# Performance work log

Hardware: AMD Instinct MI355X
Metric: run time of the kernel (lower is better)

Reference implementation:

```python
import jax, jax.numpy as jnp
import numpy as np


def setup_inputs() -> dict:
    key = jax.random.key(0)
    k0, k1, k2, k3 = jax.random.split(key, 4)
    B, S, D, F, E = 8, 2048, 1024, 2048, 8
    x = jax.random.normal(k0, (B, S, D), dtype=jnp.float32)
    Wg = jax.random.normal(k1, (D, E), dtype=jnp.float32) * 0.02
    W1 = jax.random.normal(k2, (E, D, F), dtype=jnp.float32) * 0.02
    W2 = jax.random.normal(k3, (E, F, D), dtype=jnp.float32) * 0.02
    return {"x": x, "Wg": Wg, "W1": W1, "W2": W2}


def reference(x, Wg, W1, W2):
    # Expert-choice MoE: experts pick top-C tokens, conflicts resolved by
    # max router prob (ties -> lowest expert index, matching the serial loop).
    B, S, D = x.shape
    E = Wg.shape[1]
    T = B * S
    cap = max(1, T // E)  # capacity_factor = 1.0

    xt = x.reshape(T, D)
    logits = xt @ Wg                      # [T, E]
    probs = jax.nn.softmax(logits, axis=-1)
    pT = probs.T                          # [E, T] token affinities per expert

    _, top_idx = jax.lax.top_k(pT, cap)   # [E, cap] tokens chosen by each expert
    sel = jnp.zeros((E, T), dtype=bool).at[jnp.arange(E)[:, None], top_idx].set(True)

    # Serial conflict loop is equivalent to: per token, pick the selecting
    masked = jnp.where(sel, pT, -jnp.inf)
    assigned = sel.any(axis=0)            # [T]
    tok2exp = jnp.where(assigned,
                        jnp.argmax(masked, axis=0),
                        jnp.argmax(pT, axis=0))          # [T] int
    weights = jnp.take_along_axis(probs, tok2exp[:, None], axis=1)[:, 0]  # [T]

    # Dispatch / expert FFN / weighted combine. Loop over the small fixed
    # expert set; masked tokens contribute exactly zero, matching index_add_.
    out = jnp.zeros_like(xt)
    for e in range(E):
        gate = jnp.where(tok2exp == e, weights, 0.0)     # [T]
        h = jax.nn.gelu(xt @ W1[e], approximate=False) @ W2[e]  # [T, D]
        out = out + gate[:, None] * h

    return out.reshape(B, S, D)
```

## Files before the change

### kernel.cpp

```cpp
#include <hip/hip_runtime.h>
#include <hip/hip_bf16.h>
#include <math.h>

#define T_TOK 16384
#define DIM   1024
#define FF    2048
#define NE    8
#define CAPK  2048
#define MTE_MAX 16
#define WL1SZ (NE * 8 * MTE_MAX)
#define WL2SZ (NE * 4 * MTE_MAX)

typedef unsigned short u16;
typedef unsigned long long u64;
typedef __attribute__((ext_vector_type(8))) short bf16x8;
typedef __attribute__((ext_vector_type(4))) float f32x4;

__device__ __forceinline__ u16 f2bf(float f) {
  __hip_bfloat16 h = __float2bfloat16(f);
  union { __hip_bfloat16 h; u16 u; } c; c.h = h; return c.u;
}

__device__ __forceinline__ float gelu_f(float v) {
  float z = fabsf(v) * 0.70710678118654752f;
  float t = __builtin_amdgcn_rcpf(1.0f + 0.3275911f * z);
  float poly = t * (0.254829592f +
               t * (-0.284496736f +
               t * (1.421413741f +
               t * (-1.453152027f +
               t * 1.061405429f))));
  float ez = __expf(-z * z);
  float erfz = 1.0f - poly * ez;
  erfz = copysignf(erfz, v);
  return 0.5f * v * (1.0f + erfz);
}

__device__ __forceinline__ void async_copy16(const void* g, void* l) {
  __builtin_amdgcn_global_load_lds(
      (const __attribute__((address_space(1))) unsigned int*)g,
      (__attribute__((address_space(3))) unsigned int*)l, 16, 0, 0);
}

__device__ __forceinline__ bf16x8 ds_read16(const char* p) {
  bf16x8 r;
  asm volatile("ds_read_b128 %0, %1"
               : "=&v"(r)
               : "v"((const __attribute__((address_space(3))) char*)p));
  return r;
}

__global__ __launch_bounds__(256) void transpose_cvt2(const float* __restrict__ W1,
                                                      const float* __restrict__ W2,
                                                      u16* __restrict__ w1t,
                                                      u16* __restrict__ w2t) {
  __shared__ float tile[64][65];
  int z = blockIdx.y;
  const float* src;
  u16* dst;
  int R, C;
  if (z < 8) { src = W1 + (size_t)z * DIM * FF; dst = w1t + (size_t)z * DIM * FF; R = DIM; C = FF; }
  else       { src = W2 + (size_t)(z - 8) * FF * DIM; dst = w2t + (size_t)(z - 8) * FF * DIM; R = FF; C = DIM; }
  int nbx = C >> 6;
  int bx = blockIdx.x % nbx, by = blockIdx.x / nbx;
  int r0 = by * 64, c0 = bx * 64;
  int tid = threadIdx.x;
  int lr = tid >> 4, lc4 = (tid & 15) * 4;
#pragma unroll
  for (int p = 0; p < 4; ++p) {
    float4 v = *(const float4*)(src + (size_t)(r0 + p * 16 + lr) * C + c0 + lc4);
    tile[p * 16 + lr][lc4 + 0] = v.x;
    tile[p * 16 + lr][lc4 + 1] = v.y;
    tile[p * 16 + lr][lc4 + 2] = v.z;
    tile[p * 16 + lr][lc4 + 3] = v.w;
  }
  __syncthreads();
  int oc = tid >> 3, orr = (tid & 7) * 8;
#pragma unroll
  for (int p = 0; p < 2; ++p) {
    int c = p * 32 + oc;
    u16 h[8];
#pragma unroll
    for (int j = 0; j < 8; ++j) h[j] = f2bf(tile[orr + j][c]);
    *(uint4*)(dst + (size_t)(c0 + c) * R + r0 + orr) = *(uint4*)h;
  }
}

__global__ __launch_bounds__(256) void router_k(const float* __restrict__ x,
                                                const float* __restrict__ Wg,
                                                float* __restrict__ probs,
                                                float* __restrict__ probsT,
                                                u16* __restrict__ xb,
                                                u64* __restrict__ key,
                                                int* cnt, int* cnt2) {
  int tid = threadIdx.x;
  if (tid < 4) key[blockIdx.x * 4 + tid] = 0ull;
  if (blockIdx.x == 0 && tid < NE) { cnt[tid] = 0; cnt2[tid] = 0; }
  int wid = tid >> 6, lane = tid & 63;
  int t = blockIdx.x * 4 + wid;
  const float* xr = x + (size_t)t * DIM;
  u16* xbr = xb + (size_t)t * DIM;
  double acc[NE] = {0, 0, 0, 0, 0, 0, 0, 0};
#pragma unroll 1
  for (int it = 0; it < DIM / 64; ++it) {
    int d = it * 64 + lane;
    float xv = xr[d];
    xbr[d] = f2bf(xv);
    const float4* wrow = (const float4*)(Wg + (size_t)d * NE);
    float4 w0 = wrow[0], w1 = wrow[1];
    acc[0] += (double)xv * (double)w0.x;
    acc[1] += (double)xv * (double)w0.y;
    acc[2] += (double)xv * (double)w0.z;
    acc[3] += (double)xv * (double)w0.w;
    acc[4] += (double)xv * (double)w1.x;
    acc[5] += (double)xv * (double)w1.y;
    acc[6] += (double)xv * (double)w1.z;
    acc[7] += (double)xv * (double)w1.w;
  }
#pragma unroll
  for (int e = 0; e < NE; ++e)
    for (int o = 32; o > 0; o >>= 1) acc[e] += __shfl_down(acc[e], o, 64);
  if (lane == 0) {
    float l[NE], mx = -3.0e38f;
#pragma unroll
    for (int e = 0; e < NE; ++e) { l[e] = (float)acc[e]; mx = fmaxf(mx, l[e]); }
    float s = 0.f;
#pragma unroll
    for (int e = 0; e < NE; ++e) { l[e] = expf(l[e] - mx); s += l[e]; }
    float inv = 1.0f / s;
#pragma unroll
    for (int e = 0; e < NE; ++e) {
      float p = l[e] * inv;
      probs[(size_t)t * NE + e] = p;
      probsT[(size_t)e * T_TOK + t] = p;
    }
  }
}

__global__ __launch_bounds__(256) void topk_sel(const float* __restrict__ probsT,
                                                u64* __restrict__ key) {
  __shared__ float pcol[T_TOK];
  __shared__ unsigned whist[8][2048];
  __shared__ unsigned hist[2048];
  __shared__ unsigned bcast[2];
  __shared__ unsigned wsum[4];
  __shared__ int wps[4];
  int e = blockIdx.x, tid = threadIdx.x, wid = tid >> 6, lane = tid & 63;
  const float4* src4 = (const float4*)(probsT + (size_t)e * T_TOK);
  for (int i = tid; i < T_TOK / 4; i += 256) ((float4*)pcol)[i] = src4[i];
  for (int i = tid; i < 8 * 2048; i += 256) ((unsigned*)whist)[i] = 0;
  unsigned prefix = 0, remaining = CAPK;
#pragma unroll 1
  for (int lvl = 0; lvl < 3; ++lvl) {
    int nb = (lvl == 2) ? 1024 : 2048;
    if (lvl == 0) {
      __syncthreads();
      for (int i = tid; i < T_TOK; i += 256)
        atomicAdd(&whist[wid][__float_as_uint(pcol[i]) >> 21], 1u);
      __syncthreads();
      for (int j = tid; j < 2048; j += 256) {
        unsigned s2 = 0;
#pragma unroll
        for (int w = 0; w < 8; ++w) s2 += whist[w][j];
        hist[j] = s2;
      }
      __syncthreads();
    } else {
      for (int i = tid; i < 2048; i += 256) hist[i] = 0;
      __syncthreads();
      for (int i = tid; i < T_TOK; i += 256) {
        unsigned k = __float_as_uint(pcol[i]);
        bool m = (lvl == 1) ? ((k >> 21) == prefix) : ((k >> 10) == prefix);
        if (m) atomicAdd(&hist[(lvl == 1) ? ((k >> 10) & 2047u) : (k & 1023u)], 1u);
      }
      __syncthreads();
    }
    int nper = nb / 256;
    unsigned cv = 0;
    for (int j = 0; j < nper; ++j) cv += hist[tid * nper + j];
    unsigned s = cv;
#pragma unroll
    for (int o = 1; o < 64; o <<= 1) {
      unsigned tv = __shfl_down(s, o, 64);
      if (lane + o < 64) s += tv;
    }
    if (lane == 0) wsum[wid] = s;
    __syncthreads();
    unsigned above = 0;
    for (int w = wid + 1; w < 4; ++w) above += wsum[w];
    unsigned Sincl = s + above, Sexcl = Sincl - cv;
    if (Sincl >= remaining && Sexcl < remaining) {
      unsigned rem2 = remaining - Sexcl, cum2 = 0;
      for (int j = nper - 1; j >= 0; --j) {
        unsigned h = hist[tid * nper + j];
        if (cum2 + h >= rem2) { bcast[0] = (unsigned)(tid * nper + j); bcast[1] = rem2 - cum2; break; }
        cum2 += h;
      }
    }
    __syncthreads();
    unsigned b = bcast[0];
    remaining = bcast[1];
    prefix = (lvl == 0) ? b : (lvl == 1) ? ((prefix << 11) | b) : ((prefix << 10) | b);
    __syncthreads();
  }
  unsigned vk = prefix;
  int need = (int)remaining;
  const int CH = T_TOK / 256;
  int i0 = tid * CH;
  int myt = 0;
  for (int i = i0; i < i0 + CH; ++i)
    myt += (__float_as_uint(pcol[i]) == vk);
  int p = myt;
#pragma unroll
  for (int o = 1; o < 64; o <<= 1) {
    int tv = __shfl_up(p, o, 64);
    if (lane >= o) p += tv;
  }
  if (lane == 63) wps[wid] = p;
  __syncthreads();
  int wo = 0;
  for (int w = 0; w < wid; ++w) wo += wps[w];
  int run = wo + p - myt;
  u64 ebits = (u64)(7 - e);
  for (int i = i0; i < i0 + CH; ++i) {
    unsigned k = __float_as_uint(pcol[i]);
    bool sv = false;
    if (k > vk) sv = true;
    else if (k == vk) { if (run < need) sv = true; run++; }
    if (sv) atomicMax(&key[i], ((u64)k << 3) | ebits);
  }
}

__global__ __launch_bounds__(256) void assign_k(const float* __restrict__ probs,
                                                const u64* __restrict__ key,
                                                int* __restrict__ tok2exp,
                                                float* __restrict__ wgt, int* cnt) {
  int t = blockIdx.x * 256 + threadIdx.x;
  int lane = threadIdx.x & 63;
  u64 k = key[t];
  int best;
  float bp;
  if (k) {
    best = 7 - (int)(k & 7);
    bp = __uint_as_float((unsigned)(k >> 3));
  } else {
    best = 0; bp = -3.0e38f;
#pragma unroll
    for (int e = 0; e < NE; ++e) {
      float p = probs[(size_t)t * NE + e];
      if (p > bp) { bp = p; best = e; }
    }
  }
  tok2exp[t] = best;
  wgt[t] = bp;
#pragma unroll
  for (int e = 0; e < NE; ++e) {
    u64 m = __ballot(best == e);
    if (best == e && lane == __ffsll(m) - 1) atomicAdd(&cnt[e], (int)__popcll(m));
  }
}

__global__ __launch_bounds__(256) void slot_wl_k(const int* __restrict__ tok2exp,
                                                 const int* __restrict__ cnt,
                                                 int* cnt2, int* __restrict__ list,
                                                 int* basep, int* wl1, int* wl2) {
  int gid = blockIdx.x * 256 + threadIdx.x;
  int lane = threadIdx.x & 63;
  int c[NE];
#pragma unroll
  for (int e = 0; e < NE; ++e) c[e] = cnt[e];
  if (gid < NE) {
    int r = 0;
    for (int e = 0; e < gid; ++e) r += c[e];
    basep[gid] = r;
  }
  if (gid < WL1SZ) {
    int e = gid & 7, j = gid >> 3;
    int mte = (c[e] + 255) >> 8;
    int v = -1;
    if (j < 8 * mte) {
      int half = 4 * mte;
      int h = (j >= half) ? 1 : 0;
      int jj = j - h * half;
      v = e | ((jj >> 2) << 4) | (((h << 2) | (jj & 3)) << 12);
    }
    wl1[gid] = v;
  }
  if (gid >= WL1SZ && gid < WL1SZ + WL2SZ) {
    int g2 = gid - WL1SZ;
    int e = g2 & 7, j = g2 >> 3;
    int mte = (c[e] + 255) >> 8;
    int v = -1;
    if (j < 4 * mte) {
      int half = 2 * mte;
      int h = (j >= half) ? 1 : 0;
      int jj = j - h * half;
      v = e | ((jj >> 1) << 4) | (((h << 1) | (jj & 1)) << 12);
    }
    wl2[g2] = v;
  }
  int te = tok2exp[gid];
  int bp_e = 0;
#pragma unroll
  for (int e = 0; e < NE; ++e) if (e < te) bp_e += c[e];
  int sl = 0;
#pragma unroll
  for (int e = 0; e < NE; ++e) {
    u64 m = __ballot(te == e);
    if (te == e) {
      int leader = __ffsll(m) - 1;
      int rank = __popcll(m & ((1ull << lane) - 1));
      int b = 0;
      if (lane == leader) b = atomicAdd(&cnt2[e], (int)__popcll(m));
      b = __shfl(b, leader, 64);
      sl = bp_e + b + rank;
    }
  }
  list[sl] = gid;
}


#define MF(M, N_, AV, BV) acc[M][N_] = __builtin_amdgcn_mfma_f32_16x16x32_bf16(BV, AV, acc[M][N_], 0, 0, 0)

#define SLOT_A(s) (sm + (s) * 32768)
#define SLOT_B(s) (sm + (s) * 32768 + 16384)

#define DSA_LO(s)                                                                 \
  pa = SLOT_A(s) + wr * 8192 + laneOff;                                           \
  a0 = ds_read16(pa);        a1 = ds_read16(pa + 1024);                           \
  a2 = ds_read16(pa + 2048); a3 = ds_read16(pa + 3072);

#define DSA_HI(s)                                                                 \
  pa = SLOT_A(s) + wr * 8192 + 4096 + laneOff;                                    \
  a4 = ds_read16(pa);        a5 = ds_read16(pa + 1024);                           \
  a6 = ds_read16(pa + 2048); a7 = ds_read16(pa + 3072);

#define DSB_RD(s, BP)                                                             \
  pb = SLOT_B(s) + wc * 4096 + laneOff;                                           \
  BP##0 = ds_read16(pb);        BP##1 = ds_read16(pb + 1024);                     \
  BP##2 = ds_read16(pb + 2048); BP##3 = ds_read16(pb + 3072);

#define LGKM(n)                                                                   \
  do {                                                                            \
    asm volatile("s_waitcnt lgkmcnt(" #n ")" ::: "memory");                       \
    __builtin_amdgcn_sched_barrier(0);                                            \
  } while (0)

#define VMW(n) asm volatile("s_waitcnt vmcnt(" #n ")" ::: "memory")
#define BAR() asm volatile("s_barrier" ::: "memory")

#define MFMA_LO(BP)                                                               \
  do {                                                                            \
    __builtin_amdgcn_s_setprio(1);                                                \
    MF(0, 0, a0, BP##0); MF(0, 1, a0, BP##1); MF(0, 2, a0, BP##2); MF(0, 3, a0, BP##3); \
    MF(1, 0, a1, BP##0); MF(1, 1, a1, BP##1); MF(1, 2, a1, BP##2); MF(1, 3, a1, BP##3); \
    MF(2, 0, a2, BP##0); MF(2, 1, a2, BP##1); MF(2, 2, a2, BP##2); MF(2, 3, a2, BP##3); \
    MF(3, 0, a3, BP##0); MF(3, 1, a3, BP##1); MF(3, 2, a3, BP##2); MF(3, 3, a3, BP##3); \
    __builtin_amdgcn_s_setprio(0);                                                \
  } while (0)

#define MFMA_HI(BP)                                                               \
  do {                                                                            \
    __builtin_amdgcn_s_setprio(1);                                                \
    MF(4, 0, a4, BP##0); MF(4, 1, a4, BP##1); MF(4, 2, a4, BP##2); MF(4, 3, a4, BP##3); \
    MF(5, 0, a5, BP##0); MF(5, 1, a5, BP##1); MF(5, 2, a5, BP##2); MF(5, 3, a5, BP##3); \
    MF(6, 0, a6, BP##0); MF(6, 1, a6, BP##1); MF(6, 2, a6, BP##2); MF(6, 3, a6, BP##3); \
    MF(7, 0, a7, BP##0); MF(7, 1, a7, BP##1); MF(7, 2, a7, BP##2); MF(7, 3, a7, BP##3); \
    __builtin_amdgcn_s_setprio(0);                                                \
  } while (0)

#define STAGE_A(s, kt)                                                            \
  do {                                                                            \
    async_copy16(aP0 + (size_t)(kt) * 64, SLOT_A(s) + wid * 1024);                \
    async_copy16(aP1 + (size_t)(kt) * 64, SLOT_A(s) + 8192 + wid * 1024);         \
  } while (0)

#define STAGE_B(s, kt)                                                            \
  do {                                                                            \
    async_copy16(bP0 + (size_t)(kt) * 64, SLOT_B(s) + wid * 1024);                \
    async_copy16(bP1 + (size_t)(kt) * 64, SLOT_B(s) + 8192 + wid * 1024);         \
  } while (0)

#define TILE_KT(kt, BCUR, BNXT)                                                   \
  do {                                                                            \
    const int sC = (kt) & 3, sP = ((kt) + 3) & 3, sN = ((kt) + 1) & 3;            \
    if ((kt) + 3 < KT) STAGE_A(sP, (kt) + 3);                                     \
    DSA_HI(sC);                                                                   \
    LGKM(4);                                                                      \
    MFMA_LO(BCUR);                                                                \
    if ((kt) + 3 < KT) STAGE_B(sP, (kt) + 3);                                     \
    if ((kt) < KT - 1) {                                                          \
      if ((kt) < KT - 3)        { VMW(8); }                                       \
      else if ((kt) == KT - 3)  { VMW(4); }                                       \
      else                      { VMW(0); }                                       \
      BAR();                                                                      \
      DSB_RD(sN, BNXT);                                                           \
      DSA_LO(sN);                                                                 \
      LGKM(8);                                                                    \
    } else {                                                                      \
      LGKM(0);                                                                    \
    }                                                                             \
    MFMA_HI(BCUR);                                                                \
  } while (0)

template <int EPI>
__global__ __launch_bounds__(512, 2) void ffn_k(const u16* __restrict__ A,
                                                const u16* __restrict__ Bm,
                                                void* __restrict__ Out,
                                                const int* __restrict__ list,
                                                const float* __restrict__ wgt,
                                                const int* __restrict__ basep,
                                                const int* __restrict__ cnt,
                                                const int* __restrict__ wl) {
  constexpr int K = EPI ? FF : DIM;
  constexpr int N = EPI ? DIM : FF;
  constexpr int KT = K / 32;

  const int wle = wl[blockIdx.x];
  if (wle < 0) return;
  const int e = wle & 15, mt = (wle >> 4) & 255, nt = wle >> 12;
  const int ce = cnt[e];
  const int be = basep[e];

  __shared__ u16 smem[65536];
  __shared__ int toks[256];
  __shared__ float wsc[256];
  char* const sm = (char*)smem;

  const int tid = threadIdx.x;
  if (tid < 256) {
    int r = mt * 256 + tid;
    int tk = (r < ce) ? list[be + r] : list[be];
    toks[tid] = tk;
    if (EPI == 1) wsc[tid] = wgt[tk];
  }
  __syncthreads();

  const int wid = tid >> 6, lane = tid & 63;
  const int wr = wid >> 2, wc = wid & 3;
  const int laneOff = ((lane & 15) >> 1) * 128 + (lane & 1) * 64 +
                      (((lane >> 4) << 4) ^ (((lane >> 1) & 3) << 4));

  const int tr0 = ((tid >> 3) << 1) + ((tid >> 2) & 1), tr1 = 128 + tr0;
  const int cbl = ((tid & 3) << 4) ^ (((tid >> 3) & 3) << 4);
  const char *aP0, *aP1;
  if (EPI == 0) {
    aP0 = (const char*)(A + (size_t)toks[tr0] * K) + cbl;
    aP1 = (const char*)(A + (size_t)toks[tr1] * K) + cbl;
  } else {
    aP0 = (const char*)(A + ((size_t)be + mt * 256 + tr0) * K) + cbl;
    aP1 = (const char*)(A + ((size_t)be + mt * 256 + tr1) * K) + cbl;
  }
  const char* bP0 = (const char*)(Bm + ((size_t)e * N + nt * 256 + tr0) * K) + cbl;
  const char* bP1 = (const char*)(Bm + ((size_t)e * N + nt * 256 + tr1) * K) + cbl;

  f32x4 acc[8][4];
#pragma unroll
  for (int m = 0; m < 8; ++m)
#pragma unroll
    for (int n = 0; n < 4; ++n) acc[m][n] = (f32x4){0.f, 0.f, 0.f, 0.f};

  STAGE_A(0, 0); STAGE_B(0, 0);
  STAGE_A(1, 1); STAGE_B(1, 1);
  STAGE_A(2, 2); STAGE_B(2, 2);
  VMW(8);
  BAR();

  const char* pa;
  const char* pb;
  bf16x8 a0, a1, a2, a3, a4, a5, a6, a7;
  bf16x8 bA0, bA1, bA2, bA3, bB0, bB1, bB2, bB3;

  DSB_RD(0, bA);
  DSA_LO(0);

#pragma unroll 1
  for (int kt = 0; kt < KT; kt += 2) {
    TILE_KT(kt, bA, bB);
    TILE_KT(kt + 1, bB, bA);
  }

  const int lc = lane & 15, lq = (lane >> 4) * 4;
#pragma unroll
  for (int m = 0; m < 8; ++m) {
    int trow = wr * 128 + m * 16 + lc;
    int grow = mt * 256 + trow;
    if (grow < ce) {
      if (EPI == 0) {
        size_t rowoff = (size_t)(be + grow) * FF + nt * 256 + wc * 64 + lq;
#pragma unroll
        for (int n = 0; n < 4; ++n) {
          ushort4 h4;
          h4.x = f2bf(gelu_f(acc[m][n][0]));
          h4.y = f2bf(gelu_f(acc[m][n][1]));
          h4.z = f2bf(gelu_f(acc[m][n][2]));
          h4.w = f2bf(gelu_f(acc[m][n][3]));
          *(ushort4*)((u16*)Out + rowoff + n * 16) = h4;
        }
      } else {
        float w = wsc[trow];
        size_t rowoff = (size_t)toks[trow] * DIM + nt * 256 + wc * 64 + lq;
#pragma unroll
        for (int n = 0; n < 4; ++n) {
          float4 o = make_float4(w * acc[m][n][0], w * acc[m][n][1],
                                 w * acc[m][n][2], w * acc[m][n][3]);
          *(float4*)((float*)Out + rowoff + n * 16) = o;
        }
      }
    }
  }
}

extern "C" void kernel_launch(void* const* d_in, const int* in_sizes, int n_in,
                              void* d_out, int out_size, void* d_ws, size_t ws_size,
                              hipStream_t stream) {
  (void)in_sizes; (void)n_in; (void)out_size; (void)ws_size;
  const float* x  = (const float*)d_in[0];
  const float* Wg = (const float*)d_in[1];
  const float* W1 = (const float*)d_in[2];
  const float* W2 = (const float*)d_in[3];
  float* out = (float*)d_out;

  char* ws = (char*)d_ws;
  size_t off = 0;
  auto alloc = [&](size_t bytes) -> void* {
    void* p = ws + off;
    off += (bytes + 255) & ~(size_t)255;
    return p;
  };
  u16* xb   = (u16*)alloc((size_t)T_TOK * DIM * 2);
  u16* w1t  = (u16*)alloc((size_t)NE * FF * DIM * 2);
  u16* w2t  = (u16*)alloc((size_t)NE * DIM * FF * 2);
  u16* H    = (u16*)alloc((size_t)(T_TOK + 256) * FF * 2);
  float* probs  = (float*)alloc((size_t)T_TOK * NE * 4);
  float* probsT = (float*)alloc((size_t)NE * T_TOK * 4);
  u64* key      = (u64*)alloc((size_t)T_TOK * 8);
  float* wgt    = (float*)alloc((size_t)T_TOK * 4);
  int* tok2exp  = (int*)alloc((size_t)T_TOK * 4);
  int* list     = (int*)alloc((size_t)T_TOK * 4);
  int* cnt      = (int*)alloc(64);
  int* cnt2     = (int*)alloc(64);
  int* basep    = (int*)alloc(64);
  int* wl1      = (int*)alloc(WL1SZ * 4);
  int* wl2      = (int*)alloc(WL2SZ * 4);

  transpose_cvt2<<<dim3(512, 16), 256, 0, stream>>>(W1, W2, w1t, w2t);
  router_k<<<T_TOK / 4, 256, 0, stream>>>(x, Wg, probs, probsT, xb, key, cnt, cnt2);
  topk_sel<<<NE, 256, 0, stream>>>(probsT, key);
  assign_k<<<T_TOK / 256, 256, 0, stream>>>(probs, key, tok2exp, wgt, cnt);
  slot_wl_k<<<T_TOK / 256, 256, 0, stream>>>(tok2exp, cnt, cnt2, list, basep, wl1, wl2);
  ffn_k<0><<<WL1SZ, 512, 0, stream>>>(xb, w1t, H, list, wgt, basep, cnt, wl1);
  ffn_k<1><<<WL2SZ, 512, 0, stream>>>(H, w2t, out, list, wgt, basep, cnt, wl2);
}
```

Measured before the change: 386.7 us.

## Merge prep and routing kernels, shrink FFN GEMM tiles to 128x128 double-buffered

```diff
diff --git a/kernel.cpp b/kernel.cpp
--- a/kernel.cpp
+++ b/kernel.cpp
@@ -7,9 +7,8 @@
 #define FF    2048
 #define NE    8
 #define CAPK  2048
-#define MTE_MAX 16
-#define WL1SZ (NE * 8 * MTE_MAX)
-#define WL2SZ (NE * 4 * MTE_MAX)
+#define WL1SZ 4096
+#define WL2SZ 2048
 
 typedef unsigned short u16;
 typedef unsigned long long u64;
@@ -49,361 +48,325 @@
   return r;
 }
 
-__global__ __launch_bounds__(256) void transpose_cvt2(const float* __restrict__ W1,
-                                                      const float* __restrict__ W2,
-                                                      u16* __restrict__ w1t,
-                                                      u16* __restrict__ w2t) {
+#define LGKM0()                                                                   \
+  do {                                                                            \
+    asm volatile("s_waitcnt lgkmcnt(0)" ::: "memory");                            \
+    __builtin_amdgcn_sched_barrier(0);                                            \
+  } while (0)
+#define VMW0() asm volatile("s_waitcnt vmcnt(0)" ::: "memory")
+#define BAR() asm volatile("s_barrier" ::: "memory")
+
+__global__ __launch_bounds__(256) void prep_k(const float* __restrict__ x,
+                                              const float* __restrict__ Wg,
+                                              const float* __restrict__ W1,
+                                              const float* __restrict__ W2,
+                                              float* __restrict__ probs,
+                                              float* __restrict__ probsT,
+                                              u16* __restrict__ xb,
+                                              u16* __restrict__ w1t,
+                                              u16* __restrict__ w2t,
+                                              u64* __restrict__ key,
+                                              int* cnt, int* cnt2, int* gates) {
   __shared__ float tile[64][65];
-  int z = blockIdx.y;
-  const float* src;
-  u16* dst;
-  int R, C;
-  if (z < 8) { src = W1 + (size_t)z * DIM * FF; dst = w1t + (size_t)z * DIM * FF; R = DIM; C = FF; }
-  else       { src = W2 + (size_t)(z - 8) * FF * DIM; dst = w2t + (size_t)(z - 8) * FF * DIM; R = FF; C = DIM; }
-  int nbx = C >> 6;
-  int bx = blockIdx.x % nbx, by = blockIdx.x / nbx;
-  int r0 = by * 64, c0 = bx * 64;
-  int tid = threadIdx.x;
-  int lr = tid >> 4, lc4 = (tid & 15) * 4;
-#pragma unroll
-  for (int p = 0; p < 4; ++p) {
-    float4 v = *(const float4*)(src + (size_t)(r0 + p * 16 + lr) * C + c0 + lc4);
-    tile[p * 16 + lr][lc4 + 0] = v.x;
-    tile[p * 16 + lr][lc4 + 1] = v.y;
-    tile[p * 16 + lr][lc4 + 2] = v.z;
-    tile[p * 16 + lr][lc4 + 3] = v.w;
+  int bid = blockIdx.x, tid = threadIdx.x;
+  if (bid < 4096) {
+    if (tid < 4) key[bid * 4 + tid] = 0ull;
+    if (bid == 0 && tid < NE) { cnt[tid] = 0; cnt2[tid] = 0; }
+    if (bid == 0 && tid >= 8 && tid < 10) gates[tid - 8] = 0;
+    int wid = tid >> 6, lane = tid & 63;
+    int t = bid * 4 + wid;
+    const float* xr = x + (size_t)t * DIM;
+    u16* xbr = xb + (size_t)t * DIM;
+    double acc[NE] = {0, 0, 0, 0, 0, 0, 0, 0};
+#pragma unroll 1
+    for (int it = 0; it < DIM / 64; ++it) {
+      int d = it * 64 + lane;
+      float xv = xr[d];
+      xbr[d] = f2bf(xv);
+      const float4* wrow = (const float4*)(Wg + (size_t)d * NE);
+      float4 w0 = wrow[0], w1 = wrow[1];
+      acc[0] += (double)xv * (double)w0.x;
+      acc[1] += (double)xv * (double)w0.y;
+      acc[2] += (double)xv * (double)w0.z;
+      acc[3] += (double)xv * (double)w0.w;
+      acc[4] += (double)xv * (double)w1.x;
+      acc[5] += (double)xv * (double)w1.y;
+      acc[6] += (double)xv * (double)w1.z;
+      acc[7] += (double)xv * (double)w1.w;
+    }
+#pragma unroll
+    for (int e = 0; e < NE; ++e)
+      for (int o = 32; o > 0; o >>= 1) acc[e] += __shfl_down(acc[e], o, 64);
+    if (lane == 0) {
+      float l[NE], mx = -3.0e38f;
+#pragma unroll
+      for (int e = 0; e < NE; ++e) { l[e] = (float)acc[e]; mx = fmaxf(mx, l[e]); }
+      float s = 0.f;
+#pragma unroll
+      for (int e = 0; e < NE; ++e) { l[e] = expf(l[e] - mx); s += l[e]; }
+      float inv = 1.0f / s;
+#pragma unroll
+      for (int e = 0; e < NE; ++e) {
+        float p = l[e] * inv;
+        probs[(size_t)t * NE + e] = p;
+        probsT[(size_t)e * T_TOK + t] = p;
+      }
+    }
+  } else {
+    int tz = bid - 4096;
+    int z = tz >> 9, bxy = tz & 511;
+    const float* src;
+    u16* dst;
+    int R, C;
+    if (z < 8) { src = W1 + (size_t)z * DIM * FF; dst = w1t + (size_t)z * DIM * FF; R = DIM; C = FF; }
+    else       { src = W2 + (size_t)(z - 8) * FF * DIM; dst = w2t + (size_t)(z - 8) * FF * DIM; R = FF; C = DIM; }
+    int nbx = C >> 6;
+    int bx = bxy % nbx, by = bxy / nbx;
+    int r0 = by * 64, c0 = bx * 64;
+    int lr = tid >> 4, lc4 = (tid & 15) * 4;
+#pragma unroll
+    for (int p = 0; p < 4; ++p) {
+      float4 v = *(const float4*)(src + (size_t)(r0 + p * 16 + lr) * C + c0 + lc4);
+      tile[p * 16 + lr][lc4 + 0] = v.x;
+      tile[p * 16 + lr][lc4 + 1] = v.y;
+      tile[p * 16 + lr][lc4 + 2] = v.z;
+      tile[p * 16 + lr][lc4 + 3] = v.w;
+    }
+    __syncthreads();
+    int oc = tid >> 3, orr = (tid & 7) * 8;
+#pragma unroll
+    for (int p = 0; p < 2; ++p) {
+      int c = p * 32 + oc;
+      u16 h[8];
+#pragma unroll
+      for (int j = 0; j < 8; ++j) h[j] = f2bf(tile[orr + j][c]);
+      *(uint4*)(dst + (size_t)(c0 + c) * R + r0 + orr) = *(uint4*)h;
+    }
   }
-  __syncthreads();
-  int oc = tid >> 3, orr = (tid & 7) * 8;
-#pragma unroll
-  for (int p = 0; p < 2; ++p) {
-    int c = p * 32 + oc;
-    u16 h[8];
-#pragma unroll
-    for (int j = 0; j < 8; ++j) h[j] = f2bf(tile[orr + j][c]);
-    *(uint4*)(dst + (size_t)(c0 + c) * R + r0 + orr) = *(uint4*)h;
-  }
-}
-
-__global__ __launch_bounds__(256) void router_k(const float* __restrict__ x,
-                                                const float* __restrict__ Wg,
-                                                float* __restrict__ probs,
-                                                float* __restrict__ probsT,
-                                                u16* __restrict__ xb,
-                                                u64* __restrict__ key,
-                                                int* cnt, int* cnt2) {
-  int tid = threadIdx.x;
-  if (tid < 4) key[blockIdx.x * 4 + tid] = 0ull;
-  if (blockIdx.x == 0 && tid < NE) { cnt[tid] = 0; cnt2[tid] = 0; }
-  int wid = tid >> 6, lane = tid & 63;
-  int t = blockIdx.x * 4 + wid;
-  const float* xr = x + (size_t)t * DIM;
-  u16* xbr = xb + (size_t)t * DIM;
-  double acc[NE] = {0, 0, 0, 0, 0, 0, 0, 0};
-#pragma unroll 1
-  for (int it = 0; it < DIM / 64; ++it) {
-    int d = it * 64 + lane;
-    float xv = xr[d];
-    xbr[d] = f2bf(xv);
-    const float4* wrow = (const float4*)(Wg + (size_t)d * NE);
-    float4 w0 = wrow[0], w1 = wrow[1];
-    acc[0] += (double)xv * (double)w0.x;
-    acc[1] += (double)xv * (double)w0.y;
-    acc[2] += (double)xv * (double)w0.z;
-    acc[3] += (double)xv * (double)w0.w;
-    acc[4] += (double)xv * (double)w1.x;
-    acc[5] += (double)xv * (double)w1.y;
-    acc[6] += (double)xv * (double)w1.z;
-    acc[7] += (double)xv * (double)w1.w;
-  }
-#pragma unroll
-  for (int e = 0; e < NE; ++e)
-    for (int o = 32; o > 0; o >>= 1) acc[e] += __shfl_down(acc[e], o, 64);
-  if (lane == 0) {
-    float l[NE], mx = -3.0e38f;
-#pragma unroll
-    for (int e = 0; e < NE; ++e) { l[e] = (float)acc[e]; mx = fmaxf(mx, l[e]); }
-    float s = 0.f;
-#pragma unroll
-    for (int e = 0; e < NE; ++e) { l[e] = expf(l[e] - mx); s += l[e]; }
-    float inv = 1.0f / s;
-#pragma unroll
-    for (int e = 0; e < NE; ++e) {
-      float p = l[e] * inv;
-      probs[(size_t)t * NE + e] = p;
-      probsT[(size_t)e * T_TOK + t] = p;
-    }
-  }
-}
-
-__global__ __launch_bounds__(256) void topk_sel(const float* __restrict__ probsT,
-                                                u64* __restrict__ key) {
+}
+
+__global__ __launch_bounds__(256) void moe_route_k(const float* __restrict__ probsT,
+                                                   const float* __restrict__ probs,
+                                                   u64* __restrict__ key,
+                                                   int* __restrict__ tok2exp,
+                                                   float* __restrict__ wgt,
+                                                   int* cnt, int* cnt2,
+                                                   int* __restrict__ list,
+                                                   int* basep, int* wl1, int* wl2,
+                                                   int* gates) {
   __shared__ float pcol[T_TOK];
   __shared__ unsigned whist[8][2048];
   __shared__ unsigned hist[2048];
   __shared__ unsigned bcast[2];
   __shared__ unsigned wsum[4];
   __shared__ int wps[4];
-  int e = blockIdx.x, tid = threadIdx.x, wid = tid >> 6, lane = tid & 63;
-  const float4* src4 = (const float4*)(probsT + (size_t)e * T_TOK);
-  for (int i = tid; i < T_TOK / 4; i += 256) ((float4*)pcol)[i] = src4[i];
-  for (int i = tid; i < 8 * 2048; i += 256) ((unsigned*)whist)[i] = 0;
-  unsigned prefix = 0, remaining = CAPK;
+  int bid = blockIdx.x, tid = threadIdx.x, wid = tid >> 6, lane = tid & 63;
+  if (bid < 8) {
+    int e = bid;
+    const float4* src4 = (const float4*)(probsT + (size_t)e * T_TOK);
+    for (int i = tid; i < T_TOK / 4; i += 256) ((float4*)pcol)[i] = src4[i];
+    for (int i = tid; i < 8 * 2048; i += 256) ((unsigned*)whist)[i] = 0;
+    unsigned prefix = 0, remaining = CAPK;
 #pragma unroll 1
-  for (int lvl = 0; lvl < 3; ++lvl) {
-    int nb = (lvl == 2) ? 1024 : 2048;
-    if (lvl == 0) {
+    for (int lvl = 0; lvl < 3; ++lvl) {
+      int nb = (lvl == 2) ? 1024 : 2048;
+      if (lvl == 0) {
+        __syncthreads();
+        for (int i = tid; i < T_TOK; i += 256)
+          atomicAdd(&whist[wid][__float_as_uint(pcol[i]) >> 21], 1u);
+        __syncthreads();
+        for (int j = tid; j < 2048; j += 256) {
+          unsigned s2 = 0;
+#pragma unroll
+          for (int w = 0; w < 8; ++w) s2 += whist[w][j];
+          hist[j] = s2;
+        }
+        __syncthreads();
+      } else {
+        for (int i = tid; i < 2048; i += 256) hist[i] = 0;
+        __syncthreads();
+        for (int i = tid; i < T_TOK; i += 256) {
+          unsigned k = __float_as_uint(pcol[i]);
+          bool m = (lvl == 1) ? ((k >> 21) == prefix) : ((k >> 10) == prefix);
+          if (m) atomicAdd(&hist[(lvl == 1) ? ((k >> 10) & 2047u) : (k & 1023u)], 1u);
+        }
+        __syncthreads();
+      }
+      int nper = nb / 256;
+      unsigned cv = 0;
+      for (int j = 0; j < nper; ++j) cv += hist[tid * nper + j];
+      unsigned s = cv;
+#pragma unroll
+      for (int o = 1; o < 64; o <<= 1) {
+        unsigned tv = __shfl_down(s, o, 64);
+        if (lane + o < 64) s += tv;
+      }
+      if (lane == 0) wsum[wid] = s;
       __syncthreads();
-      for (int i = tid; i < T_TOK; i += 256)
-        atomicAdd(&whist[wid][__float_as_uint(pcol[i]) >> 21], 1u);
+      unsigned above = 0;
+      for (int w = wid + 1; w < 4; ++w) above += wsum[w];
+      unsigned Sincl = s + above, Sexcl = Sincl - cv;
+      if (Sincl >= remaining && Sexcl < remaining) {
+        unsigned rem2 = remaining - Sexcl, cum2 = 0;
+        for (int j = nper - 1; j >= 0; --j) {
+          unsigned h = hist[tid * nper + j];
+          if (cum2 + h >= rem2) { bcast[0] = (unsigned)(tid * nper + j); bcast[1] = rem2 - cum2; break; }
+          cum2 += h;
+        }
+      }
       __syncthreads();
-      for (int j = tid; j < 2048; j += 256) {
-        unsigned s2 = 0;
-#pragma unroll
-        for (int w = 0; w < 8; ++w) s2 += whist[w][j];
-        hist[j] = s2;
-      }
+      unsigned b = bcast[0];
+      remaining = bcast[1];
+      prefix = (lvl == 0) ? b : (lvl == 1) ? ((prefix << 11) | b) : ((prefix << 10) | b);
       __syncthreads();
+    }
+    unsigned vk = prefix;
+    int need = (int)remaining;
+    const int CH = T_TOK / 256;
+    int i0 = tid * CH;
+    int myt = 0;
+    for (int i = i0; i < i0 + CH; ++i)
+      myt += (__float_as_uint(pcol[i]) == vk);
+    int p = myt;
+#pragma unroll
+    for (int o = 1; o < 64; o <<= 1) {
+      int tv = __shfl_up(p, o, 64);
+      if (lane >= o) p += tv;
+    }
+    if (lane == 63) wps[wid] = p;
+    __syncthreads();
+    int wo = 0;
+    for (int w = 0; w < wid; ++w) wo += wps[w];
+    int run = wo + p - myt;
+    u64 ebits = (u64)(7 - e);
+    for (int i = i0; i < i0 + CH; ++i) {
+      unsigned k = __float_as_uint(pcol[i]);
+      bool sv = false;
+      if (k > vk) sv = true;
+      else if (k == vk) { if (run < need) sv = true; run++; }
+      if (sv) atomicMax(&key[i], ((u64)k << 3) | ebits);
+    }
+    __threadfence();
+    __syncthreads();
+    if (tid == 0) atomicAdd(&gates[0], 1);
+  } else if (bid < 72) {
+    if (tid == 0) {
+      while (atomicAdd(&gates[0], 0) < 8) __builtin_amdgcn_s_sleep(8);
+    }
+    __syncthreads();
+    __threadfence();
+    int t = (bid - 8) * 256 + tid;
+    u64 k = key[t];
+    int best;
+    float bp;
+    if (k) {
+      best = 7 - (int)(k & 7);
+      bp = __uint_as_float((unsigned)(k >> 3));
     } else {
-      for (int i = tid; i < 2048; i += 256) hist[i] = 0;
-      __syncthreads();
-      for (int i = tid; i < T_TOK; i += 256) {
-        unsigned k = __float_as_uint(pcol[i]);
-        bool m = (lvl == 1) ? ((k >> 21) == prefix) : ((k >> 10) == prefix);
-        if (m) atomicAdd(&hist[(lvl == 1) ? ((k >> 10) & 2047u) : (k & 1023u)], 1u);
-      }
-      __syncthreads();
-    }
-    int nper = nb / 256;
-    unsigned cv = 0;
-    for (int j = 0; j < nper; ++j) cv += hist[tid * nper + j];
-    unsigned s = cv;
-#pragma unroll
-    for (int o = 1; o < 64; o <<= 1) {
-      unsigned tv = __shfl_down(s, o, 64);
-      if (lane + o < 64) s += tv;
-    }
-    if (lane == 0) wsum[wid] = s;
+      best = 0; bp = -3.0e38f;
+#pragma unroll
+      for (int e = 0; e < NE; ++e) {
+        float p = probs[(size_t)t * NE + e];
+        if (p > bp) { bp = p; best = e; }
+      }
+    }
+    tok2exp[t] = best;
+    wgt[t] = bp;
+#pragma unroll
+    for (int e = 0; e < NE; ++e) {
+      u64 m = __ballot(best == e);
+      if (best == e && lane == __ffsll(m) - 1) atomicAdd(&cnt[e], (int)__popcll(m));
+    }
+    __threadfence();
     __syncthreads();
-    unsigned above = 0;
-    for (int w = wid + 1; w < 4; ++w) above += wsum[w];
-    unsigned Sincl = s + above, Sexcl = Sincl - cv;
-    if (Sincl >= remaining && Sexcl < remaining) {
-      unsigned rem2 = remaining - Sexcl, cum2 = 0;
-      for (int j = nper - 1; j >= 0; --j) {
-        unsigned h = hist[tid * nper + j];
-        if (cum2 + h >= rem2) { bcast[0] = (unsigned)(tid * nper + j); bcast[1] = rem2 - cum2; break; }
-        cum2 += h;
-      }
+    if (tid == 0) atomicAdd(&gates[1], 1);
+  } else {
+    if (tid == 0) {
+      while (atomicAdd(&gates[1], 0) < 64) __builtin_amdgcn_s_sleep(8);
     }
     __syncthreads();
-    unsigned b = bcast[0];
-    remaining = bcast[1];
-    prefix = (lvl == 0) ? b : (lvl == 1) ? ((prefix << 11) | b) : ((prefix << 10) | b);
-    __syncthreads();
+    __threadfence();
+    int gid = (bid - 72) * 256 + tid;
+    int c[NE];
+#pragma unroll
+    for (int e = 0; e < NE; ++e) c[e] = cnt[e];
+    if (gid < NE) {
+      int r = 0;
+      for (int e = 0; e < gid; ++e) r += c[e];
+      basep[gid] = r;
+    }
+    if (gid < WL1SZ) {
+      int e = gid & 7, j = gid >> 3;
+      int mte = (c[e] + 127) >> 7;
+      wl1[gid] = (j < mte * 16) ? (e | ((j >> 4) << 4) | ((j & 15) << 12)) : -1;
+    }
+    if (gid >= WL1SZ && gid < WL1SZ + WL2SZ) {
+      int g2 = gid - WL1SZ;
+      int e = g2 & 7, j = g2 >> 3;
+      int mte = (c[e] + 127) >> 7;
+      wl2[g2] = (j < mte * 8) ? (e | ((j >> 3) << 4) | ((j & 7) << 12)) : -1;
+    }
+    int te = tok2exp[gid];
+    int bp_e = 0;
+#pragma unroll
+    for (int e = 0; e < NE; ++e) if (e < te) bp_e += c[e];
+    int sl = 0;
+#pragma unroll
+    for (int e = 0; e < NE; ++e) {
+      u64 m = __ballot(te == e);
+      if (te == e) {
+        int leader = __ffsll(m) - 1;
+        int rank = __popcll(m & ((1ull << lane) - 1));
+        int b = 0;
+        if (lane == leader) b = atomicAdd(&cnt2[e], (int)__popcll(m));
+        b = __shfl(b, leader, 64);
+        sl = bp_e + b + rank;
+      }
+    }
+    list[sl] = gid;
   }
-  unsigned vk = prefix;
-  int need = (int)remaining;
-  const int CH = T_TOK / 256;
-  int i0 = tid * CH;
-  int myt = 0;
-  for (int i = i0; i < i0 + CH; ++i)
-    myt += (__float_as_uint(pcol[i]) == vk);
-  int p = myt;
-#pragma unroll
-  for (int o = 1; o < 64; o <<= 1) {
-    int tv = __shfl_up(p, o, 64);
-    if (lane >= o) p += tv;
-  }
-  if (lane == 63) wps[wid] = p;
-  __syncthreads();
-  int wo = 0;
-  for (int w = 0; w < wid; ++w) wo += wps[w];
-  int run = wo + p - myt;
-  u64 ebits = (u64)(7 - e);
-  for (int i = i0; i < i0 + CH; ++i) {
-    unsigned k = __float_as_uint(pcol[i]);
-    bool sv = false;
-    if (k > vk) sv = true;
-    else if (k == vk) { if (run < need) sv = true; run++; }
-    if (sv) atomicMax(&key[i], ((u64)k << 3) | ebits);
-  }
-}
-
-__global__ __launch_bounds__(256) void assign_k(const float* __restrict__ probs,
-                                                const u64* __restrict__ key,
-                                                int* __restrict__ tok2exp,
-                                                float* __restrict__ wgt, int* cnt) {
-  int t = blockIdx.x * 256 + threadIdx.x;
-  int lane = threadIdx.x & 63;
-  u64 k = key[t];
-  int best;
-  float bp;
-  if (k) {
-    best = 7 - (int)(k & 7);
-    bp = __uint_as_float((unsigned)(k >> 3));
-  } else {
-    best = 0; bp = -3.0e38f;
-#pragma unroll
-    for (int e = 0; e < NE; ++e) {
-      float p = probs[(size_t)t * NE + e];
-      if (p > bp) { bp = p; best = e; }
-    }
-  }
-  tok2exp[t] = best;
-  wgt[t] = bp;
-#pragma unroll
-  for (int e = 0; e < NE; ++e) {
-    u64 m = __ballot(best == e);
-    if (best == e && lane == __ffsll(m) - 1) atomicAdd(&cnt[e], (int)__popcll(m));
-  }
-}
-
-__global__ __launch_bounds__(256) void slot_wl_k(const int* __restrict__ tok2exp,
-                                                 const int* __restrict__ cnt,
-                                                 int* cnt2, int* __restrict__ list,
-                                                 int* basep, int* wl1, int* wl2) {
-  int gid = blockIdx.x * 256 + threadIdx.x;
-  int lane = threadIdx.x & 63;
-  int c[NE];
-#pragma unroll
-  for (int e = 0; e < NE; ++e) c[e] = cnt[e];
-  if (gid < NE) {
-    int r = 0;
-    for (int e = 0; e < gid; ++e) r += c[e];
-    basep[gid] = r;
-  }
-  if (gid < WL1SZ) {
-    int e = gid & 7, j = gid >> 3;
-    int mte = (c[e] + 255) >> 8;
-    int v = -1;
-    if (j < 8 * mte) {
-      int half = 4 * mte;
-      int h = (j >= half) ? 1 : 0;
-      int jj = j - h * half;
-      v = e | ((jj >> 2) << 4) | (((h << 2) | (jj & 3)) << 12);
-    }
-    wl1[gid] = v;
-  }
-  if (gid >= WL1SZ && gid < WL1SZ + WL2SZ) {
-    int g2 = gid - WL1SZ;
-    int e = g2 & 7, j = g2 >> 3;
-    int mte = (c[e] + 255) >> 8;
-    int v = -1;
-    if (j < 4 * mte) {
-      int half = 2 * mte;
-      int h = (j >= half) ? 1 : 0;
-      int jj = j - h * half;
-      v = e | ((jj >> 1) << 4) | (((h << 1) | (jj & 1)) << 12);
-    }
-    wl2[g2] = v;
-  }
-  int te = tok2exp[gid];
-  int bp_e = 0;
-#pragma unroll
-  for (int e = 0; e < NE; ++e) if (e < te) bp_e += c[e];
-  int sl = 0;
-#pragma unroll
-  for (int e = 0; e < NE; ++e) {
-    u64 m = __ballot(te == e);
-    if (te == e) {
-      int leader = __ffsll(m) - 1;
-      int rank = __popcll(m & ((1ull << lane) - 1));
-      int b = 0;
-      if (lane == leader) b = atomicAdd(&cnt2[e], (int)__popcll(m));
-      b = __shfl(b, leader, 64);
-      sl = bp_e + b + rank;
-    }
-  }
-  list[sl] = gid;
 }
 
 
 #define MF(M, N_, AV, BV) acc[M][N_] = __builtin_amdgcn_mfma_f32_16x16x32_bf16(BV, AV, acc[M][N_], 0, 0, 0)
 
-#define SLOT_A(s) (sm + (s) * 32768)
-#define SLOT_B(s) (sm + (s) * 32768 + 16384)
-
-#define DSA_LO(s)                                                                 \
-  pa = SLOT_A(s) + wr * 8192 + laneOff;                                           \
-  a0 = ds_read16(pa);        a1 = ds_read16(pa + 1024);                           \
-  a2 = ds_read16(pa + 2048); a3 = ds_read16(pa + 3072);
-
-#define DSA_HI(s)                                                                 \
-  pa = SLOT_A(s) + wr * 8192 + 4096 + laneOff;                                    \
-  a4 = ds_read16(pa);        a5 = ds_read16(pa + 1024);                           \
-  a6 = ds_read16(pa + 2048); a7 = ds_read16(pa + 3072);
-
-#define DSB_RD(s, BP)                                                             \
-  pb = SLOT_B(s) + wc * 4096 + laneOff;                                           \
-  BP##0 = ds_read16(pb);        BP##1 = ds_read16(pb + 1024);                     \
-  BP##2 = ds_read16(pb + 2048); BP##3 = ds_read16(pb + 3072);
-
-#define LGKM(n)                                                                   \
+#define STG(b, kt)                                                                \
   do {                                                                            \
-    asm volatile("s_waitcnt lgkmcnt(" #n ")" ::: "memory");                       \
-    __builtin_amdgcn_sched_barrier(0);                                            \
+    char* dA = sm + (b) * 32768;                                                  \
+    char* dB = dA + 16384;                                                        \
+    size_t ko = (size_t)(kt) * 128;                                               \
+    async_copy16(aP0 + ko,      dA + tid * 16);                                   \
+    async_copy16(aP1 + ko,      dA + 4096 + tid * 16);                            \
+    async_copy16(aP0 + ko + 64, dA + 8192 + tid * 16);                            \
+    async_copy16(aP1 + ko + 64, dA + 12288 + tid * 16);                           \
+    async_copy16(bP0 + ko,      dB + tid * 16);                                   \
+    async_copy16(bP1 + ko,      dB + 4096 + tid * 16);                            \
+    async_copy16(bP0 + ko + 64, dB + 8192 + tid * 16);                            \
+    async_copy16(bP1 + ko + 64, dB + 12288 + tid * 16);                           \
   } while (0)
 
-#define VMW(n) asm volatile("s_waitcnt vmcnt(" #n ")" ::: "memory")
-#define BAR() asm volatile("s_barrier" ::: "memory")
-
-#define MFMA_LO(BP)                                                               \
+#define DSRD(kkoff)                                                               \
+  do {                                                                            \
+    const char* pa = sm + bb * 32768 + (kkoff) + wr * 4096 + laneOff;             \
+    const char* pb = sm + bb * 32768 + 16384 + (kkoff) + wc * 4096 + laneOff;     \
+    a0 = ds_read16(pa);        a1 = ds_read16(pa + 1024);                         \
+    a2 = ds_read16(pa + 2048); a3 = ds_read16(pa + 3072);                         \
+    b0 = ds_read16(pb);        b1 = ds_read16(pb + 1024);                         \
+    b2 = ds_read16(pb + 2048); b3 = ds_read16(pb + 3072);                         \
+  } while (0)
+
+#define MFMA16()                                                                  \
   do {                                                                            \
     __builtin_amdgcn_s_setprio(1);                                                \
-    MF(0, 0, a0, BP##0); MF(0, 1, a0, BP##1); MF(0, 2, a0, BP##2); MF(0, 3, a0, BP##3); \
-    MF(1, 0, a1, BP##0); MF(1, 1, a1, BP##1); MF(1, 2, a1, BP##2); MF(1, 3, a1, BP##3); \
-    MF(2, 0, a2, BP##0); MF(2, 1, a2, BP##1); MF(2, 2, a2, BP##2); MF(2, 3, a2, BP##3); \
-    MF(3, 0, a3, BP##0); MF(3, 1, a3, BP##1); MF(3, 2, a3, BP##2); MF(3, 3, a3, BP##3); \
+    MF(0, 0, a0, b0); MF(0, 1, a0, b1); MF(0, 2, a0, b2); MF(0, 3, a0, b3);       \
+    MF(1, 0, a1, b0); MF(1, 1, a1, b1); MF(1, 2, a1, b2); MF(1, 3, a1, b3);       \
+    MF(2, 0, a2, b0); MF(2, 1, a2, b1); MF(2, 2, a2, b2); MF(2, 3, a2, b3);       \
+    MF(3, 0, a3, b0); MF(3, 1, a3, b1); MF(3, 2, a3, b2); MF(3, 3, a3, b3);       \
     __builtin_amdgcn_s_setprio(0);                                                \
   } while (0)
 
-#define MFMA_HI(BP)                                                               \
-  do {                                                                            \
-    __builtin_amdgcn_s_setprio(1);                                                \
-    MF(4, 0, a4, BP##0); MF(4, 1, a4, BP##1); MF(4, 2, a4, BP##2); MF(4, 3, a4, BP##3); \
-    MF(5, 0, a5, BP##0); MF(5, 1, a5, BP##1); MF(5, 2, a5, BP##2); MF(5, 3, a5, BP##3); \
-    MF(6, 0, a6, BP##0); MF(6, 1, a6, BP##1); MF(6, 2, a6, BP##2); MF(6, 3, a6, BP##3); \
-    MF(7, 0, a7, BP##0); MF(7, 1, a7, BP##1); MF(7, 2, a7, BP##2); MF(7, 3, a7, BP##3); \
-    __builtin_amdgcn_s_setprio(0);                                                \
-  } while (0)
-
-#define STAGE_A(s, kt)                                                            \
-  do {                                                                            \
-    async_copy16(aP0 + (size_t)(kt) * 64, SLOT_A(s) + wid * 1024);                \
-    async_copy16(aP1 + (size_t)(kt) * 64, SLOT_A(s) + 8192 + wid * 1024);         \
-  } while (0)
-
-#define STAGE_B(s, kt)                                                            \
-  do {                                                                            \
-    async_copy16(bP0 + (size_t)(kt) * 64, SLOT_B(s) + wid * 1024);                \
-    async_copy16(bP1 + (size_t)(kt) * 64, SLOT_B(s) + 8192 + wid * 1024);         \
-  } while (0)
-
-#define TILE_KT(kt, BCUR, BNXT)                                                   \
-  do {                                                                            \
-    const int sC = (kt) & 3, sP = ((kt) + 3) & 3, sN = ((kt) + 1) & 3;            \
-    if ((kt) + 3 < KT) STAGE_A(sP, (kt) + 3);                                     \
-    DSA_HI(sC);                                                                   \
-    LGKM(4);                                                                      \
-    MFMA_LO(BCUR);                                                                \
-    if ((kt) + 3 < KT) STAGE_B(sP, (kt) + 3);                                     \
-    if ((kt) < KT - 1) {                                                          \
-      if ((kt) < KT - 3)        { VMW(8); }                                       \
-      else if ((kt) == KT - 3)  { VMW(4); }                                       \
-      else                      { VMW(0); }                                       \
-      BAR();                                                                      \
-      DSB_RD(sN, BNXT);                                                           \
-      DSA_LO(sN);                                                                 \
-      LGKM(8);                                                                    \
-    } else {                                                                      \
-      LGKM(0);                                                                    \
-    }                                                                             \
-    MFMA_HI(BCUR);                                                                \
-  } while (0)
-
 template <int EPI>
-__global__ __launch_bounds__(512, 2) void ffn_k(const u16* __restrict__ A,
+__global__ __launch_bounds__(256, 2) void ffn_k(const u16* __restrict__ A,
                                                 const u16* __restrict__ Bm,
                                                 void* __restrict__ Out,
                                                 const int* __restrict__ list,
@@ -413,7 +376,7 @@
                                                 const int* __restrict__ wl) {
   constexpr int K = EPI ? FF : DIM;
   constexpr int N = EPI ? DIM : FF;
-  constexpr int KT = K / 32;
+  constexpr int KT = K / 64;
 
   const int wle = wl[blockIdx.x];
   if (wle < 0) return;
@@ -421,14 +384,14 @@
   const int ce = cnt[e];
   const int be = basep[e];
 
-  __shared__ u16 smem[65536];
-  __shared__ int toks[256];
-  __shared__ float wsc[256];
+  __shared__ u16 smem[32768];
+  __shared__ int toks[128];
+  __shared__ float wsc[128];
   char* const sm = (char*)smem;
 
   const int tid = threadIdx.x;
-  if (tid < 256) {
-    int r = mt * 256 + tid;
+  if (tid < 128) {
+    int r = mt * 128 + tid;
     int tk = (r < ce) ? list[be + r] : list[be];
     toks[tid] = tk;
     if (EPI == 1) wsc[tid] = wgt[tk];
@@ -436,57 +399,57 @@
   __syncthreads();
 
   const int wid = tid >> 6, lane = tid & 63;
-  const int wr = wid >> 2, wc = wid & 3;
+  const int wr = wid >> 1, wc = wid & 1;
   const int laneOff = ((lane & 15) >> 1) * 128 + (lane & 1) * 64 +
-                      (((lane >> 4) << 4) ^ (((lane >> 1) & 3) << 4));
-
-  const int tr0 = ((tid >> 3) << 1) + ((tid >> 2) & 1), tr1 = 128 + tr0;
+                      (((lane >> 4) << 4) ^ ((((lane & 15) >> 1) & 3) << 4));
+
+  const int r0 = 2 * (tid >> 3) + ((tid & 7) >> 2);
   const int cbl = ((tid & 3) << 4) ^ (((tid >> 3) & 3) << 4);
   const char *aP0, *aP1;
   if (EPI == 0) {
-    aP0 = (const char*)(A + (size_t)toks[tr0] * K) + cbl;
-    aP1 = (const char*)(A + (size_t)toks[tr1] * K) + cbl;
+    aP0 = (const char*)(A + (size_t)toks[r0] * K) + cbl;
+    aP1 = (const char*)(A + (size_t)toks[r0 + 64] * K) + cbl;
   } else {
-    aP0 = (const char*)(A + ((size_t)be + mt * 256 + tr0) * K) + cbl;
-    aP1 = (const char*)(A + ((size_t)be + mt * 256 + tr1) * K) + cbl;
+    aP0 = (const char*)(A + ((size_t)be + mt * 128 + r0) * K) + cbl;
+    aP1 = (const char*)(A + ((size_t)be + mt * 128 + r0 + 64) * K) + cbl;
   }
-  const char* bP0 = (const char*)(Bm + ((size_t)e * N + nt * 256 + tr0) * K) + cbl;
-  const char* bP1 = (const char*)(Bm + ((size_t)e * N + nt * 256 + tr1) * K) + cbl;
-
-  f32x4 acc[8][4];
-#pragma unroll
-  for (int m = 0; m < 8; ++m)
+  const char* bP0 = (const char*)(Bm + ((size_t)e * N + nt * 128 + r0) * K) + cbl;
+  const char* bP1 = (const char*)(Bm + ((size_t)e * N + nt * 128 + r0 + 64) * K) + cbl;
+
+  f32x4 acc[4][4];
+#pragma unroll
+  for (int m = 0; m < 4; ++m)
 #pragma unroll
     for (int n = 0; n < 4; ++n) acc[m][n] = (f32x4){0.f, 0.f, 0.f, 0.f};
 
-  STAGE_A(0, 0); STAGE_B(0, 0);
-  STAGE_A(1, 1); STAGE_B(1, 1);
-  STAGE_A(2, 2); STAGE_B(2, 2);
-  VMW(8);
+  STG(0, 0);
+  VMW0();
   BAR();
 
-  const char* pa;
-  const char* pb;
-  bf16x8 a0, a1, a2, a3, a4, a5, a6, a7;
-  bf16x8 bA0, bA1, bA2, bA3, bB0, bB1, bB2, bB3;
-
-  DSB_RD(0, bA);
-  DSA_LO(0);
+  bf16x8 a0, a1, a2, a3, b0, b1, b2, b3;
 
 #pragma unroll 1
-  for (int kt = 0; kt < KT; kt += 2) {
-    TILE_KT(kt, bA, bB);
-    TILE_KT(kt + 1, bB, bA);
+  for (int kt = 0; kt < KT; ++kt) {
+    const int bb = kt & 1;
+    if (kt + 1 < KT) STG(bb ^ 1, kt + 1);
+    DSRD(0);
+    LGKM0();
+    MFMA16();
+    DSRD(8192);
+    LGKM0();
+    MFMA16();
+    VMW0();
+    BAR();
   }
 
   const int lc = lane & 15, lq = (lane >> 4) * 4;
 #pragma unroll
-  for (int m = 0; m < 8; ++m) {
-    int trow = wr * 128 + m * 16 + lc;
-    int grow = mt * 256 + trow;
+  for (int m = 0; m < 4; ++m) {
+    int trow = wr * 64 + m * 16 + lc;
+    int grow = mt * 128 + trow;
     if (grow < ce) {
       if (EPI == 0) {
-        size_t rowoff = (size_t)(be + grow) * FF + nt * 256 + wc * 64 + lq;
+        size_t rowoff = (size_t)(be + grow) * FF + nt * 128 + wc * 64 + lq;
 #pragma unroll
         for (int n = 0; n < 4; ++n) {
           ushort4 h4;
@@ -498,7 +461,7 @@
         }
       } else {
         float w = wsc[trow];
-        size_t rowoff = (size_t)toks[trow] * DIM + nt * 256 + wc * 64 + lq;
+        size_t rowoff = (size_t)toks[trow] * DIM + nt * 128 + wc * 64 + lq;
 #pragma unroll
         for (int n = 0; n < 4; ++n) {
           float4 o = make_float4(w * acc[m][n][0], w * acc[m][n][1],
@@ -540,14 +503,14 @@
   int* cnt      = (int*)alloc(64);
   int* cnt2     = (int*)alloc(64);
   int* basep    = (int*)alloc(64);
+  int* gates    = (int*)alloc(64);
   int* wl1      = (int*)alloc(WL1SZ * 4);
   int* wl2      = (int*)alloc(WL2SZ * 4);
 
-  transpose_cvt2<<<dim3(512, 16), 256, 0, stream>>>(W1, W2, w1t, w2t);
-  router_k<<<T_TOK / 4, 256, 0, stream>>>(x, Wg, probs, probsT, xb, key, cnt, cnt2);
-  topk_sel<<<NE, 256, 0, stream>>>(probsT, key);
-  assign_k<<<T_TOK / 256, 256, 0, stream>>>(probs, key, tok2exp, wgt, cnt);
-  slot_wl_k<<<T_TOK / 256, 256, 0, stream>>>(tok2exp, cnt, cnt2, list, basep, wl1, wl2);
-  ffn_k<0><<<WL1SZ, 512, 0, stream>>>(xb, w1t, H, list, wgt, basep, cnt, wl1);
-  ffn_k<1><<<WL2SZ, 512, 0, stream>>>(H, w2t, out, list, wgt, basep, cnt, wl2);
-}
+  prep_k<<<4096 + 8192, 256, 0, stream>>>(x, Wg, W1, W2, probs, probsT, xb, w1t, w2t,
+                                          key, cnt, cnt2, gates);
+  moe_route_k<<<136, 256, 0, stream>>>(probsT, probs, key, tok2exp, wgt, cnt, cnt2,
+                                       list, basep, wl1, wl2, gates);
+  ffn_k<0><<<WL1SZ, 256, 0, stream>>>(xb, w1t, H, list, wgt, basep, cnt, wl1);
+  ffn_k<1><<<WL2SZ, 256, 0, stream>>>(H, w2t, out, list, wgt, basep, cnt, wl2);
+}
```

New measurement: 376.7 us. -2.6%, faster.
